# Performance work log

Measured on AMD Instinct MI355X. Metric: run time of the kernel, lower is better.

## Reference

```python
import jax, jax.numpy as jnp
import numpy as np

D_MODEL = 1024
N_HEADS = 16
D_K = D_MODEL // N_HEADS
B, S = 2, 2048


def setup_inputs() -> dict:
    key = jax.random.key(0)
    ks = jax.random.split(key, 5)
    x = jax.random.normal(ks[0], (B, S, D_MODEL), dtype=jnp.float32)
    # causal 0/1 mask, broadcastable over batch and heads
    mask = jnp.tril(jnp.ones((S, S), dtype=jnp.int32))[None, None, :, :]
    scale = 1.0 / np.sqrt(D_MODEL)
    w_qkv_w = jax.random.normal(ks[1], (3 * D_MODEL, D_MODEL), dtype=jnp.float32) * scale
    w_qkv_b = jnp.zeros((3 * D_MODEL,), dtype=jnp.float32)
    w_o_w = jax.random.normal(ks[2], (D_MODEL, D_MODEL), dtype=jnp.float32) * scale
    w_o_b = jnp.zeros((D_MODEL,), dtype=jnp.float32)
    return {"x": x, "mask": mask, "w_qkv_w": w_qkv_w, "w_qkv_b": w_qkv_b,
            "w_o_w": w_o_w, "w_o_b": w_o_b}


def reference(x, mask, w_qkv_w, w_qkv_b, w_o_w, w_o_b):
    b, s, d = x.shape
    qkv = x @ w_qkv_w.T + w_qkv_b                       # [b, s, 3d]
    q, k, v = jnp.split(qkv, 3, axis=-1)
    # [b, h, s, dk]
    q = q.reshape(b, s, N_HEADS, D_K).transpose(0, 2, 1, 3)
    k = k.reshape(b, s, N_HEADS, D_K).transpose(0, 2, 1, 3)
    v = v.reshape(b, s, N_HEADS, D_K).transpose(0, 2, 1, 3)
    scores = jnp.einsum('bhqd,bhkd->bhqk', q, k) / jnp.sqrt(jnp.float32(D_K))
    scores = jnp.where(mask == 0, jnp.float32(-1e9), scores)
    attn = jax.nn.softmax(scores, axis=-1)
    out = jnp.einsum('bhqk,bhkd->bhqd', attn, v)        # [b, h, s, dk]
    out = out.transpose(0, 2, 1, 3).reshape(b, s, d)
    return out @ w_o_w.T + w_o_b
```

## Files before the change

kernel.cpp:

```cpp
#include <hip/hip_runtime.h>
#include <cstdint>
#include <cstddef>


typedef __attribute__((ext_vector_type(8))) short bf16x8;
typedef __attribute__((ext_vector_type(4))) float f32x4;
typedef __attribute__((ext_vector_type(4))) unsigned int u32x4;
typedef __attribute__((ext_vector_type(4))) unsigned short u16x4;
typedef __attribute__((ext_vector_type(8))) unsigned short u16x8;

__device__ __forceinline__ unsigned short f2b(float f) {
  unsigned int u = __float_as_uint(f);
  u = u + 0x7FFFu + ((u >> 16) & 1u);
  return (unsigned short)(u >> 16);
}
__device__ __forceinline__ unsigned short f2b_trunc(float f) {
  return (unsigned short)(__float_as_uint(f) >> 16);
}

__device__ __forceinline__ void gl_lds16(const unsigned short* g, unsigned short* s) {
  __builtin_amdgcn_global_load_lds((const __attribute__((address_space(1))) void*)g,
                                   (__attribute__((address_space(3))) void*)s, 16, 0, 0);
}

__global__ __launch_bounds__(256) void cvt_all(const float* __restrict__ x,
                                               const float* __restrict__ wq,
                                               const float* __restrict__ wo,
                                               unsigned short* __restrict__ xb,
                                               unsigned short* __restrict__ wqb,
                                               unsigned short* __restrict__ wob) {
  const int bid = blockIdx.x;
  const float* in;
  unsigned short* out;
  int base;
  if (bid < 4096)      { in = x;  out = xb;  base = bid; }
  else if (bid < 7168) { in = wq; out = wqb; base = bid - 4096; }
  else                 { in = wo; out = wob; base = bid - 7168; }
  const int idx = (base * 256 + threadIdx.x) * 4;
  f32x4 v = *(const f32x4*)(in + idx);
  u16x4 r;
  r[0] = f2b(v[0]); r[1] = f2b(v[1]); r[2] = f2b(v[2]); r[3] = f2b(v[3]);
  *(u16x4*)(out + idx) = r;
}

__global__ __launch_bounds__(256) void gemm_bt(const unsigned short* __restrict__ A,
                                               const unsigned short* __restrict__ W,
                                               const float* __restrict__ bias,
                                               unsigned short* __restrict__ Cb,
                                               int M, int N, int K, int qcols) {
  __shared__ unsigned short As[2][128 * 32];
  __shared__ unsigned short Bs[2][128 * 32];
  const int tid  = threadIdx.x;
  const int lane = tid & 63;
  const int w    = tid >> 6;
  const int wy   = w >> 1, wx = w & 1;
  const int l15  = lane & 15, quad = lane >> 4;
  const int xr2  = (l15 >> 1) & 3;
  const int m0 = blockIdx.y * 128, n0 = blockIdx.x * 128;

  const unsigned short* gA[2];
  const unsigned short* gB[2];
  int off[2];
#pragma unroll
  for (int p = 0; p < 2; ++p) {
    const int c = tid + p * 256;
    const int r = c >> 2;
    const int srcc = (c & 3) ^ ((r >> 1) & 3);
    gA[p] = A + (size_t)(m0 + r) * K + srcc * 8;
    gB[p] = W + (size_t)(n0 + r) * K + srcc * 8;
    off[p] = c * 8;
  }

  f32x4 acc[4][4];
#pragma unroll
  for (int i = 0; i < 4; ++i)
#pragma unroll
    for (int j = 0; j < 4; ++j) acc[i][j] = (f32x4){0.f, 0.f, 0.f, 0.f};

#pragma unroll
  for (int p = 0; p < 2; ++p) {
    gl_lds16(gA[p], &As[0][off[p]]);
    gl_lds16(gB[p], &Bs[0][off[p]]);
  }

  const int NIT = K >> 5;
  for (int it = 0; it < NIT; ++it) {
    __syncthreads();
    const int cur = it & 1;
    if (it + 1 < NIT) {
      const int kt = (it + 1) << 5;
#pragma unroll
      for (int p = 0; p < 2; ++p) {
        gl_lds16(gA[p] + kt, &As[cur ^ 1][off[p]]);
        gl_lds16(gB[p] + kt, &Bs[cur ^ 1][off[p]]);
      }
    }
    const unsigned short* Ac = As[cur];
    const unsigned short* Bc = Bs[cur];
    bf16x8 af[4], bfr[4];
#pragma unroll
    for (int i = 0; i < 4; ++i)
      af[i] = *(const bf16x8*)&Ac[(wy * 64 + i * 16 + l15) * 32 + (quad ^ xr2) * 8];
#pragma unroll
    for (int j = 0; j < 4; ++j)
      bfr[j] = *(const bf16x8*)&Bc[(wx * 64 + j * 16 + l15) * 32 + (quad ^ xr2) * 8];
#pragma unroll
    for (int i = 0; i < 4; ++i)
#pragma unroll
      for (int j = 0; j < 4; ++j)
        acc[i][j] = __builtin_amdgcn_mfma_f32_16x16x32_bf16(af[i], bfr[j], acc[i][j], 0, 0, 0);
  }

#pragma unroll
  for (int i = 0; i < 4; ++i) {
    const int row = m0 + wy * 64 + i * 16 + quad * 4;
#pragma unroll
    for (int j = 0; j < 4; ++j) {
      const int col = n0 + wx * 64 + j * 16 + l15;
      const float bv = bias[col];
      const float sc = (col < qcols) ? 0.125f : 1.0f;
#pragma unroll
      for (int r = 0; r < 4; ++r)
        Cb[(size_t)(row + r) * N + col] = f2b((acc[i][j][r] + bv) * sc);
    }
  }
}

__global__ __launch_bounds__(256) void gemm_bt64(const unsigned short* __restrict__ A,
                                                 const unsigned short* __restrict__ W,
                                                 const float* __restrict__ bias,
                                                 float* __restrict__ Cf,
                                                 int M, int N, int K) {
  __shared__ unsigned short As[2][64 * 32];
  __shared__ unsigned short Bs[2][64 * 32];
  const int tid  = threadIdx.x;
  const int lane = tid & 63;
  const int w    = tid >> 6;
  const int wy   = w >> 1, wx = w & 1;
  const int l15  = lane & 15, quad = lane >> 4;
  const int xr2  = (l15 >> 1) & 3;
  const int m0 = blockIdx.y * 64, n0 = blockIdx.x * 64;

  const unsigned short* gA0;
  const unsigned short* gB0;
  int off0;
  {
    const int c = tid;
    const int r = c >> 2;
    const int srcc = (c & 3) ^ ((r >> 1) & 3);
    gA0 = A + (size_t)(m0 + r) * K + srcc * 8;
    gB0 = W + (size_t)(n0 + r) * K + srcc * 8;
    off0 = c * 8;
  }

  f32x4 acc[2][2];
#pragma unroll
  for (int i = 0; i < 2; ++i)
#pragma unroll
    for (int j = 0; j < 2; ++j) acc[i][j] = (f32x4){0.f, 0.f, 0.f, 0.f};

  gl_lds16(gA0, &As[0][off0]);
  gl_lds16(gB0, &Bs[0][off0]);

  const int NIT = K >> 5;
  for (int it = 0; it < NIT; ++it) {
    __syncthreads();
    const int cur = it & 1;
    if (it + 1 < NIT) {
      const int kt = (it + 1) << 5;
      gl_lds16(gA0 + kt, &As[cur ^ 1][off0]);
      gl_lds16(gB0 + kt, &Bs[cur ^ 1][off0]);
    }
    const unsigned short* Ac = As[cur];
    const unsigned short* Bc = Bs[cur];
    bf16x8 af[2], bfr[2];
#pragma unroll
    for (int i = 0; i < 2; ++i)
      af[i] = *(const bf16x8*)&Ac[(wy * 32 + i * 16 + l15) * 32 + (quad ^ xr2) * 8];
#pragma unroll
    for (int j = 0; j < 2; ++j)
      bfr[j] = *(const bf16x8*)&Bc[(wx * 32 + j * 16 + l15) * 32 + (quad ^ xr2) * 8];
#pragma unroll
    for (int i = 0; i < 2; ++i)
#pragma unroll
      for (int j = 0; j < 2; ++j)
        acc[i][j] = __builtin_amdgcn_mfma_f32_16x16x32_bf16(af[i], bfr[j], acc[i][j], 0, 0, 0);
  }

#pragma unroll
  for (int i = 0; i < 2; ++i) {
    const int row = m0 + wy * 32 + i * 16 + quad * 4;
#pragma unroll
    for (int j = 0; j < 2; ++j) {
      const int col = n0 + wx * 32 + j * 16 + l15;
      const float bv = bias[col];
#pragma unroll
      for (int r = 0; r < 4; ++r)
        Cf[(size_t)(row + r) * N + col] = acc[i][j][r] + bv;
    }
  }
}

__global__ __launch_bounds__(256) void transpose_v(const unsigned short* __restrict__ qkv,
                                                   unsigned short* __restrict__ vt) {
  __shared__ unsigned short tile[64][72];
  const int tid = threadIdx.x;
  const int bh = blockIdx.y, b = bh >> 4, h = bh & 15;
  const int s0 = blockIdx.x * 64;
  const int i = tid >> 2;
  const int j = (tid & 3) * 16;
  const unsigned short* g = qkv + (size_t)(b * 2048 + s0 + i) * 3072 + 2048 + h * 64 + j;
  *(u32x4*)&tile[i][j]     = *(const u32x4*)g;
  *(u32x4*)&tile[i][j + 8] = *(const u32x4*)(g + 8);
  __syncthreads();
  const int d  = tid >> 2;
  const int sj = (tid & 3) * 16;
  u16x8 o0, o1;
#pragma unroll
  for (int k = 0; k < 8; ++k) { o0[k] = tile[sj + k][d]; o1[k] = tile[sj + 8 + k][d]; }
  unsigned short* gout = vt + (size_t)(bh * 64 + d) * 2048 + s0 + sj;
  *(u16x8*)gout       = o0;
  *(u16x8*)(gout + 8) = o1;
}

__global__ __launch_bounds__(64, 2) void attn_fwd(const unsigned short* __restrict__ qkv,
                                                  const unsigned short* __restrict__ vt,
                                                  unsigned short* __restrict__ o) {
  __shared__ unsigned short Ks[2][64 * 64];
  __shared__ unsigned short P[16 * 72];
  const int lane = threadIdx.x;
  const int l15 = lane & 15, quad = lane >> 4;
  const int xr = l15 & 7;
  const int bh = blockIdx.x, b = bh >> 4, h = bh & 15;
  const int qt = 63 - (int)blockIdx.y;
  const int q0 = qt * 32;
  const int T = (qt >> 1) + 1;

  const unsigned short* gK[8];
#pragma unroll
  for (int p = 0; p < 8; ++p) {
    const int c = p * 64 + lane;
    const int r = c >> 3;
    const int sc = ((c & 7) ^ (r & 7)) * 8;
    gK[p] = qkv + (size_t)(b * 2048 + r) * 3072 + 1024 + h * 64 + sc;
  }

  const unsigned short* qr0 = qkv + (size_t)(b * 2048 + q0 + l15) * 3072 + h * 64;
  const unsigned short* qr1 = qr0 + (size_t)16 * 3072;
  const bf16x8 bq[2][2] = {
    { *(const bf16x8*)(qr0 + quad * 8), *(const bf16x8*)(qr0 + 32 + quad * 8) },
    { *(const bf16x8*)(qr1 + quad * 8), *(const bf16x8*)(qr1 + 32 + quad * 8) } };

  const unsigned short* gV = vt + (size_t)(bh * 64) * 2048;

  bf16x8 vones;
#pragma unroll
  for (int k = 0; k < 8; ++k) vones[k] = (short)0x3F80;

  f32x4 acc[2][4];
#pragma unroll
  for (int i = 0; i < 2; ++i)
#pragma unroll
    for (int j = 0; j < 4; ++j) acc[i][j] = (f32x4){0.f, 0.f, 0.f, 0.f};
  f32x4 accL[2] = {(f32x4){0.f, 0.f, 0.f, 0.f}, (f32x4){0.f, 0.f, 0.f, 0.f}};

#pragma unroll
  for (int p = 0; p < 8; ++p) gl_lds16(gK[p], &Ks[0][p * 512]);

  for (int t = 0; t < T; ++t) {
    __syncthreads();
    const int cur = t & 1;
    const int kv0 = t * 64;
    bf16x8 av[4][2];
#pragma unroll
    for (int j = 0; j < 4; ++j) {
      const unsigned short* vrow = gV + (size_t)(j * 16 + l15) * 2048 + kv0;
      av[j][0] = *(const bf16x8*)(vrow + quad * 8);
      av[j][1] = *(const bf16x8*)(vrow + 32 + quad * 8);
    }
    if (t + 1 < T) {
      const size_t ko = (size_t)(t + 1) * 64 * 3072;
#pragma unroll
      for (int p = 0; p < 8; ++p) gl_lds16(gK[p] + ko, &Ks[cur ^ 1][p * 512]);
    }
    const unsigned short* Kc = Ks[cur];
    bf16x8 kA[4][2];
#pragma unroll
    for (int n = 0; n < 4; ++n) {
      const int row = n * 16 + l15;
      kA[n][0] = *(const bf16x8*)&Kc[row * 64 + ((quad) ^ xr) * 8];
      kA[n][1] = *(const bf16x8*)&Kc[row * 64 + ((4 + quad) ^ xr) * 8];
    }
#pragma unroll
    for (int qs = 0; qs < 2; ++qs) {
      f32x4 st[4];
#pragma unroll
      for (int n = 0; n < 4; ++n) {
        f32x4 z = (f32x4){0.f, 0.f, 0.f, 0.f};
        z = __builtin_amdgcn_mfma_f32_16x16x32_bf16(kA[n][0], bq[qs][0], z, 0, 0, 0);
        z = __builtin_amdgcn_mfma_f32_16x16x32_bf16(kA[n][1], bq[qs][1], z, 0, 0, 0);
        st[n] = z;
      }
      const int qbase = q0 + qs * 16;
      if (kv0 + 63 > qbase) {
        const int qrow = qbase + l15;
#pragma unroll
        for (int n = 0; n < 4; ++n)
#pragma unroll
          for (int r = 0; r < 4; ++r)
            if (kv0 + n * 16 + quad * 4 + r > qrow) st[n][r] = -1e30f;
      }
#pragma unroll
      for (int n = 0; n < 4; ++n) {
#pragma unroll
        for (int r = 0; r < 4; ++r) st[n][r] = __expf(st[n][r]);
        u16x4 pw;
        pw[0] = f2b_trunc(st[n][0]); pw[1] = f2b_trunc(st[n][1]);
        pw[2] = f2b_trunc(st[n][2]); pw[3] = f2b_trunc(st[n][3]);
        *(u16x4*)&P[l15 * 72 + n * 16 + quad * 4] = pw;
      }
      const bf16x8 bp0 = *(const bf16x8*)&P[l15 * 72 + quad * 8];
      const bf16x8 bp1 = *(const bf16x8*)&P[l15 * 72 + 32 + quad * 8];
      accL[qs] = __builtin_amdgcn_mfma_f32_16x16x32_bf16(vones, bp0, accL[qs], 0, 0, 0);
      accL[qs] = __builtin_amdgcn_mfma_f32_16x16x32_bf16(vones, bp1, accL[qs], 0, 0, 0);
#pragma unroll
      for (int j = 0; j < 4; ++j) {
        acc[qs][j] = __builtin_amdgcn_mfma_f32_16x16x32_bf16(av[j][0], bp0, acc[qs][j], 0, 0, 0);
        acc[qs][j] = __builtin_amdgcn_mfma_f32_16x16x32_bf16(av[j][1], bp1, acc[qs][j], 0, 0, 0);
      }
    }
  }
#pragma unroll
  for (int qs = 0; qs < 2; ++qs) {
    const int qrow = q0 + qs * 16 + l15;
    const float inv = 1.0f / accL[qs][0];
    unsigned short* orow = o + (size_t)(b * 2048 + qrow) * 1024 + h * 64;
#pragma unroll
    for (int j = 0; j < 4; ++j) {
      u16x4 ov;
      ov[0] = f2b(acc[qs][j][0] * inv); ov[1] = f2b(acc[qs][j][1] * inv);
      ov[2] = f2b(acc[qs][j][2] * inv); ov[3] = f2b(acc[qs][j][3] * inv);
      *(u16x4*)(orow + j * 16 + quad * 4) = ov;
    }
  }
}

extern "C" void kernel_launch(void* const* d_in, const int* in_sizes, int n_in,
                              void* d_out, int out_size, void* d_ws, size_t ws_size,
                              hipStream_t stream) {
  const float* x       = (const float*)d_in[0];
  const float* w_qkv_w = (const float*)d_in[2];
  const float* w_qkv_b = (const float*)d_in[3];
  const float* w_o_w   = (const float*)d_in[4];
  const float* w_o_b   = (const float*)d_in[5];
  float* out = (float*)d_out;

  unsigned short* ws    = (unsigned short*)d_ws;
  unsigned short* xb    = ws;
  unsigned short* wqb   = xb   + (size_t)4096 * 1024;
  unsigned short* wob   = wqb  + (size_t)3072 * 1024;
  unsigned short* qkvb  = wob  + (size_t)1024 * 1024;
  unsigned short* vtb   = qkvb + (size_t)4096 * 3072;
  unsigned short* attnb = vtb  + (size_t)2048 * 2048;

  cvt_all<<<8192, 256, 0, stream>>>(x, w_qkv_w, w_o_w, xb, wqb, wob);
  gemm_bt<<<dim3(24, 32), 256, 0, stream>>>(xb, wqb, w_qkv_b, qkvb, 4096, 3072, 1024, 1024);
  transpose_v<<<dim3(32, 32), 256, 0, stream>>>(qkvb, vtb);
  attn_fwd<<<dim3(32, 64), 64, 0, stream>>>(qkvb, vtb, attnb);
  gemm_bt64<<<dim3(16, 64), 256, 0, stream>>>(attnb, wob, w_o_b, out, 4096, 1024, 1024);
}
```

Before: 201.6 us.

## Software-pipeline QK^T scores one tile ahead of softmax and PV

Restructures the attention KV loop so the QK^T MFMAs for tile t are issued in the same iteration as the exp/P-write/PV MFMAs for tile t-1. This lets the scheduler overlap matrix work with the exp and LDS traffic of the previous tile. The loop runs one extra iteration and carries 32 extra float registers for the held-over scores, which raises register pressure and may lower occupancy. The V loads are also shifted to the lagged tile.

Measured after the change: 204.6 us. No clear change (+1.5%).

```diff
diff --git a/kernel.cpp b/kernel.cpp
--- a/kernel.cpp
+++ b/kernel.cpp
@@ -264,70 +264,89 @@
     for (int j = 0; j < 4; ++j) acc[i][j] = (f32x4){0.f, 0.f, 0.f, 0.f};
   f32x4 accL[2] = {(f32x4){0.f, 0.f, 0.f, 0.f}, (f32x4){0.f, 0.f, 0.f, 0.f}};
 
+  f32x4 st_old[2][4];
+
 #pragma unroll
   for (int p = 0; p < 8; ++p) gl_lds16(gK[p], &Ks[0][p * 512]);
 
-  for (int t = 0; t < T; ++t) {
+  for (int t = 0; t <= T; ++t) {
     __syncthreads();
     const int cur = t & 1;
-    const int kv0 = t * 64;
+    const bool have_cur = (t < T);
+    const bool have_def = (t >= 1);
+    const int kv0p = (t - 1) * 64;
+
     bf16x8 av[4][2];
-#pragma unroll
-    for (int j = 0; j < 4; ++j) {
-      const unsigned short* vrow = gV + (size_t)(j * 16 + l15) * 2048 + kv0;
-      av[j][0] = *(const bf16x8*)(vrow + quad * 8);
-      av[j][1] = *(const bf16x8*)(vrow + 32 + quad * 8);
+    if (have_def) {
+#pragma unroll
+      for (int j = 0; j < 4; ++j) {
+        const unsigned short* vrow = gV + (size_t)(j * 16 + l15) * 2048 + kv0p;
+        av[j][0] = *(const bf16x8*)(vrow + quad * 8);
+        av[j][1] = *(const bf16x8*)(vrow + 32 + quad * 8);
+      }
     }
     if (t + 1 < T) {
       const size_t ko = (size_t)(t + 1) * 64 * 3072;
 #pragma unroll
       for (int p = 0; p < 8; ++p) gl_lds16(gK[p] + ko, &Ks[cur ^ 1][p * 512]);
     }
-    const unsigned short* Kc = Ks[cur];
-    bf16x8 kA[4][2];
-#pragma unroll
-    for (int n = 0; n < 4; ++n) {
-      const int row = n * 16 + l15;
-      kA[n][0] = *(const bf16x8*)&Kc[row * 64 + ((quad) ^ xr) * 8];
-      kA[n][1] = *(const bf16x8*)&Kc[row * 64 + ((4 + quad) ^ xr) * 8];
-    }
-#pragma unroll
-    for (int qs = 0; qs < 2; ++qs) {
-      f32x4 st[4];
+    f32x4 stn[2][4];
+    if (have_cur) {
+      const unsigned short* Kc = Ks[cur];
+      bf16x8 kA[4][2];
 #pragma unroll
       for (int n = 0; n < 4; ++n) {
-        f32x4 z = (f32x4){0.f, 0.f, 0.f, 0.f};
-        z = __builtin_amdgcn_mfma_f32_16x16x32_bf16(kA[n][0], bq[qs][0], z, 0, 0, 0);
-        z = __builtin_amdgcn_mfma_f32_16x16x32_bf16(kA[n][1], bq[qs][1], z, 0, 0, 0);
-        st[n] = z;
+        const int row = n * 16 + l15;
+        kA[n][0] = *(const bf16x8*)&Kc[row * 64 + ((quad) ^ xr) * 8];
+        kA[n][1] = *(const bf16x8*)&Kc[row * 64 + ((4 + quad) ^ xr) * 8];
       }
-      const int qbase = q0 + qs * 16;
-      if (kv0 + 63 > qbase) {
-        const int qrow = qbase + l15;
-#pragma unroll
-        for (int n = 0; n < 4; ++n)
-#pragma unroll
-          for (int r = 0; r < 4; ++r)
-            if (kv0 + n * 16 + quad * 4 + r > qrow) st[n][r] = -1e30f;
+#pragma unroll
+      for (int qs = 0; qs < 2; ++qs)
+#pragma unroll
+        for (int n = 0; n < 4; ++n) {
+          f32x4 z = (f32x4){0.f, 0.f, 0.f, 0.f};
+          z = __builtin_amdgcn_mfma_f32_16x16x32_bf16(kA[n][0], bq[qs][0], z, 0, 0, 0);
+          z = __builtin_amdgcn_mfma_f32_16x16x32_bf16(kA[n][1], bq[qs][1], z, 0, 0, 0);
+          stn[qs][n] = z;
+        }
+    }
+    if (have_def) {
+#pragma unroll
+      for (int qs = 0; qs < 2; ++qs) {
+        const int qbase = q0 + qs * 16;
+        if (kv0p + 63 > qbase) {
+          const int qrow = qbase + l15;
+#pragma unroll
+          for (int n = 0; n < 4; ++n)
+#pragma unroll
+            for (int r = 0; r < 4; ++r)
+              if (kv0p + n * 16 + quad * 4 + r > qrow) st_old[qs][n][r] = -1e30f;
+        }
+#pragma unroll
+        for (int n = 0; n < 4; ++n) {
+#pragma unroll
+          for (int r = 0; r < 4; ++r) st_old[qs][n][r] = __expf(st_old[qs][n][r]);
+          u16x4 pw;
+          pw[0] = f2b_trunc(st_old[qs][n][0]); pw[1] = f2b_trunc(st_old[qs][n][1]);
+          pw[2] = f2b_trunc(st_old[qs][n][2]); pw[3] = f2b_trunc(st_old[qs][n][3]);
+          *(u16x4*)&P[l15 * 72 + n * 16 + quad * 4] = pw;
+        }
+        const bf16x8 bp0 = *(const bf16x8*)&P[l15 * 72 + quad * 8];
+        const bf16x8 bp1 = *(const bf16x8*)&P[l15 * 72 + 32 + quad * 8];
+        accL[qs] = __builtin_amdgcn_mfma_f32_16x16x32_bf16(vones, bp0, accL[qs], 0, 0, 0);
+        accL[qs] = __builtin_amdgcn_mfma_f32_16x16x32_bf16(vones, bp1, accL[qs], 0, 0, 0);
+#pragma unroll
+        for (int j = 0; j < 4; ++j) {
+          acc[qs][j] = __builtin_amdgcn_mfma_f32_16x16x32_bf16(av[j][0], bp0, acc[qs][j], 0, 0, 0);
+          acc[qs][j] = __builtin_amdgcn_mfma_f32_16x16x32_bf16(av[j][1], bp1, acc[qs][j], 0, 0, 0);
+        }
       }
-#pragma unroll
-      for (int n = 0; n < 4; ++n) {
-#pragma unroll
-        for (int r = 0; r < 4; ++r) st[n][r] = __expf(st[n][r]);
-        u16x4 pw;
-        pw[0] = f2b_trunc(st[n][0]); pw[1] = f2b_trunc(st[n][1]);
-        pw[2] = f2b_trunc(st[n][2]); pw[3] = f2b_trunc(st[n][3]);
-        *(u16x4*)&P[l15 * 72 + n * 16 + quad * 4] = pw;
-      }
-      const bf16x8 bp0 = *(const bf16x8*)&P[l15 * 72 + quad * 8];
-      const bf16x8 bp1 = *(const bf16x8*)&P[l15 * 72 + 32 + quad * 8];
-      accL[qs] = __builtin_amdgcn_mfma_f32_16x16x32_bf16(vones, bp0, accL[qs], 0, 0, 0);
-      accL[qs] = __builtin_amdgcn_mfma_f32_16x16x32_bf16(vones, bp1, accL[qs], 0, 0, 0);
-#pragma unroll
-      for (int j = 0; j < 4; ++j) {
-        acc[qs][j] = __builtin_amdgcn_mfma_f32_16x16x32_bf16(av[j][0], bp0, acc[qs][j], 0, 0, 0);
-        acc[qs][j] = __builtin_amdgcn_mfma_f32_16x16x32_bf16(av[j][1], bp1, acc[qs][j], 0, 0, 0);
-      }
+    }
+    if (have_cur) {
+#pragma unroll
+      for (int qs = 0; qs < 2; ++qs)
+#pragma unroll
+        for (int n = 0; n < 4; ++n) st_old[qs][n] = stn[qs][n];
     }
   }
 #pragma unroll
```

## Fuse V transpose into QKV GEMM epilogue and split attention KV across warps

Applied to the files above, without the earlier changes.

The QKV GEMM epilogue now writes V blocks directly in transposed layout, which removes the separate transpose kernel launch and its extra memory pass. The attention kernel goes from one wave per block to four waves. Each wave handles a strided subset of KV tiles and loads K straight from global memory instead of through double-buffered LDS. Partial accumulators and row sums are then reduced through shared memory. This is meant to add parallelism and hide latency for causal query tiles, at the cost of uncoalesced K loads and a reduction step.

Result: slower. 223.6 us (+10.9%).

```diff
diff --git a/kernel.cpp b/kernel.cpp
--- a/kernel.cpp
+++ b/kernel.cpp
@@ -47,6 +47,7 @@
                                                const unsigned short* __restrict__ W,
                                                const float* __restrict__ bias,
                                                unsigned short* __restrict__ Cb,
+                                               unsigned short* __restrict__ vtb,
                                                int M, int N, int K, int qcols) {
   __shared__ unsigned short As[2][128 * 32];
   __shared__ unsigned short Bs[2][128 * 32];
@@ -111,6 +112,7 @@
         acc[i][j] = __builtin_amdgcn_mfma_f32_16x16x32_bf16(af[i], bfr[j], acc[i][j], 0, 0, 0);
   }
 
+  const bool vblock = (n0 >= 2048);
 #pragma unroll
   for (int i = 0; i < 4; ++i) {
     const int row = m0 + wy * 64 + i * 16 + quad * 4;
@@ -118,10 +120,19 @@
     for (int j = 0; j < 4; ++j) {
       const int col = n0 + wx * 64 + j * 16 + l15;
       const float bv = bias[col];
-      const float sc = (col < qcols) ? 0.125f : 1.0f;
-#pragma unroll
-      for (int r = 0; r < 4; ++r)
-        Cb[(size_t)(row + r) * N + col] = f2b((acc[i][j][r] + bv) * sc);
+      if (!vblock) {
+        const float sc = (col < qcols) ? 0.125f : 1.0f;
+#pragma unroll
+        for (int r = 0; r < 4; ++r)
+          Cb[(size_t)(row + r) * N + col] = f2b((acc[i][j][r] + bv) * sc);
+      } else {
+        const int hd = col - 2048;
+        const int bb = row >> 11, s = row & 2047;
+        u16x4 ov;
+#pragma unroll
+        for (int r = 0; r < 4; ++r) ov[r] = f2b(acc[i][j][r] + bv);
+        *(u16x4*)(vtb + ((size_t)(bb * 1024 + hd)) * 2048 + s) = ov;
+      }
     }
   }
 }
@@ -201,49 +212,19 @@
   }
 }
 
-__global__ __launch_bounds__(256) void transpose_v(const unsigned short* __restrict__ qkv,
-                                                   unsigned short* __restrict__ vt) {
-  __shared__ unsigned short tile[64][72];
-  const int tid = threadIdx.x;
-  const int bh = blockIdx.y, b = bh >> 4, h = bh & 15;
-  const int s0 = blockIdx.x * 64;
-  const int i = tid >> 2;
-  const int j = (tid & 3) * 16;
-  const unsigned short* g = qkv + (size_t)(b * 2048 + s0 + i) * 3072 + 2048 + h * 64 + j;
-  *(u32x4*)&tile[i][j]     = *(const u32x4*)g;
-  *(u32x4*)&tile[i][j + 8] = *(const u32x4*)(g + 8);
-  __syncthreads();
-  const int d  = tid >> 2;
-  const int sj = (tid & 3) * 16;
-  u16x8 o0, o1;
-#pragma unroll
-  for (int k = 0; k < 8; ++k) { o0[k] = tile[sj + k][d]; o1[k] = tile[sj + 8 + k][d]; }
-  unsigned short* gout = vt + (size_t)(bh * 64 + d) * 2048 + s0 + sj;
-  *(u16x8*)gout       = o0;
-  *(u16x8*)(gout + 8) = o1;
-}
-
-__global__ __launch_bounds__(64, 2) void attn_fwd(const unsigned short* __restrict__ qkv,
-                                                  const unsigned short* __restrict__ vt,
-                                                  unsigned short* __restrict__ o) {
-  __shared__ unsigned short Ks[2][64 * 64];
-  __shared__ unsigned short P[16 * 72];
-  const int lane = threadIdx.x;
-  const int l15 = lane & 15, quad = lane >> 4;
-  const int xr = l15 & 7;
+__global__ __launch_bounds__(256, 3) void attn_fwd(const unsigned short* __restrict__ qkv,
+                                                   const unsigned short* __restrict__ vt,
+                                                   unsigned short* __restrict__ o) {
+  __shared__ unsigned short pbuf[4][16 * 72];
+  __shared__ f32x4 red[3][64][10];
+  const int tid  = threadIdx.x;
+  const int lane = tid & 63;
+  const int w    = tid >> 6;
+  const int l15  = lane & 15, quad = lane >> 4;
   const int bh = blockIdx.x, b = bh >> 4, h = bh & 15;
   const int qt = 63 - (int)blockIdx.y;
   const int q0 = qt * 32;
   const int T = (qt >> 1) + 1;
-
-  const unsigned short* gK[8];
-#pragma unroll
-  for (int p = 0; p < 8; ++p) {
-    const int c = p * 64 + lane;
-    const int r = c >> 3;
-    const int sc = ((c & 7) ^ (r & 7)) * 8;
-    gK[p] = qkv + (size_t)(b * 2048 + r) * 3072 + 1024 + h * 64 + sc;
-  }
 
   const unsigned short* qr0 = qkv + (size_t)(b * 2048 + q0 + l15) * 3072 + h * 64;
   const unsigned short* qr1 = qr0 + (size_t)16 * 3072;
@@ -251,6 +232,7 @@
     { *(const bf16x8*)(qr0 + quad * 8), *(const bf16x8*)(qr0 + 32 + quad * 8) },
     { *(const bf16x8*)(qr1 + quad * 8), *(const bf16x8*)(qr1 + 32 + quad * 8) } };
 
+  const unsigned short* gK = qkv + (size_t)(b * 2048) * 3072 + 1024 + h * 64;
   const unsigned short* gV = vt + (size_t)(bh * 64) * 2048;
 
   bf16x8 vones;
@@ -264,32 +246,23 @@
     for (int j = 0; j < 4; ++j) acc[i][j] = (f32x4){0.f, 0.f, 0.f, 0.f};
   f32x4 accL[2] = {(f32x4){0.f, 0.f, 0.f, 0.f}, (f32x4){0.f, 0.f, 0.f, 0.f}};
 
-#pragma unroll
-  for (int p = 0; p < 8; ++p) gl_lds16(gK[p], &Ks[0][p * 512]);
-
-  for (int t = 0; t < T; ++t) {
-    __syncthreads();
-    const int cur = t & 1;
+  unsigned short* P = pbuf[w];
+
+  for (int t = w; t < T; t += 4) {
     const int kv0 = t * 64;
+    bf16x8 kA[4][2];
+#pragma unroll
+    for (int n = 0; n < 4; ++n) {
+      const unsigned short* krow = gK + (size_t)(kv0 + n * 16 + l15) * 3072;
+      kA[n][0] = *(const bf16x8*)(krow + quad * 8);
+      kA[n][1] = *(const bf16x8*)(krow + 32 + quad * 8);
+    }
     bf16x8 av[4][2];
 #pragma unroll
     for (int j = 0; j < 4; ++j) {
       const unsigned short* vrow = gV + (size_t)(j * 16 + l15) * 2048 + kv0;
       av[j][0] = *(const bf16x8*)(vrow + quad * 8);
       av[j][1] = *(const bf16x8*)(vrow + 32 + quad * 8);
-    }
-    if (t + 1 < T) {
-      const size_t ko = (size_t)(t + 1) * 64 * 3072;
-#pragma unroll
-      for (int p = 0; p < 8; ++p) gl_lds16(gK[p] + ko, &Ks[cur ^ 1][p * 512]);
-    }
-    const unsigned short* Kc = Ks[cur];
-    bf16x8 kA[4][2];
-#pragma unroll
-    for (int n = 0; n < 4; ++n) {
-      const int row = n * 16 + l15;
-      kA[n][0] = *(const bf16x8*)&Kc[row * 64 + ((quad) ^ xr) * 8];
-      kA[n][1] = *(const bf16x8*)&Kc[row * 64 + ((4 + quad) ^ xr) * 8];
     }
 #pragma unroll
     for (int qs = 0; qs < 2; ++qs) {
@@ -330,17 +303,44 @@
       }
     }
   }
-#pragma unroll
-  for (int qs = 0; qs < 2; ++qs) {
-    const int qrow = q0 + qs * 16 + l15;
-    const float inv = 1.0f / accL[qs][0];
-    unsigned short* orow = o + (size_t)(b * 2048 + qrow) * 1024 + h * 64;
-#pragma unroll
-    for (int j = 0; j < 4; ++j) {
-      u16x4 ov;
-      ov[0] = f2b(acc[qs][j][0] * inv); ov[1] = f2b(acc[qs][j][1] * inv);
-      ov[2] = f2b(acc[qs][j][2] * inv); ov[3] = f2b(acc[qs][j][3] * inv);
-      *(u16x4*)(orow + j * 16 + quad * 4) = ov;
+
+  if (w > 0) {
+    f32x4* dst = red[w - 1][lane];
+#pragma unroll
+    for (int qs = 0; qs < 2; ++qs)
+#pragma unroll
+      for (int j = 0; j < 4; ++j) dst[qs * 4 + j] = acc[qs][j];
+    dst[8] = (f32x4){accL[0][0], accL[1][0], 0.f, 0.f};
+  }
+  __syncthreads();
+  if (w == 0) {
+#pragma unroll
+    for (int p = 0; p < 3; ++p) {
+      const f32x4* src = red[p][lane];
+#pragma unroll
+      for (int qs = 0; qs < 2; ++qs)
+#pragma unroll
+        for (int j = 0; j < 4; ++j) {
+          const f32x4 s = src[qs * 4 + j];
+#pragma unroll
+          for (int r = 0; r < 4; ++r) acc[qs][j][r] += s[r];
+        }
+      const f32x4 ls = src[8];
+      accL[0][0] += ls[0];
+      accL[1][0] += ls[1];
+    }
+#pragma unroll
+    for (int qs = 0; qs < 2; ++qs) {
+      const int qrow = q0 + qs * 16 + l15;
+      const float inv = 1.0f / accL[qs][0];
+      unsigned short* orow = o + (size_t)(b * 2048 + qrow) * 1024 + h * 64;
+#pragma unroll
+      for (int j = 0; j < 4; ++j) {
+        u16x4 ov;
+        ov[0] = f2b(acc[qs][j][0] * inv); ov[1] = f2b(acc[qs][j][1] * inv);
+        ov[2] = f2b(acc[qs][j][2] * inv); ov[3] = f2b(acc[qs][j][3] * inv);
+        *(u16x4*)(orow + j * 16 + quad * 4) = ov;
+      }
     }
   }
 }
@@ -364,8 +364,7 @@
   unsigned short* attnb = vtb  + (size_t)2048 * 2048;
 
   cvt_all<<<8192, 256, 0, stream>>>(x, w_qkv_w, w_o_w, xb, wqb, wob);
-  gemm_bt<<<dim3(24, 32), 256, 0, stream>>>(xb, wqb, w_qkv_b, qkvb, 4096, 3072, 1024, 1024);
-  transpose_v<<<dim3(32, 32), 256, 0, stream>>>(qkvb, vtb);
-  attn_fwd<<<dim3(32, 64), 64, 0, stream>>>(qkvb, vtb, attnb);
+  gemm_bt<<<dim3(24, 32), 256, 0, stream>>>(xb, wqb, w_qkv_b, qkvb, vtb, 4096, 3072, 1024, 1024);
+  attn_fwd<<<dim3(32, 64), 256, 0, stream>>>(qkvb, vtb, attnb);
   gemm_bt64<<<dim3(16, 64), 256, 0, stream>>>(attnb, wob, w_o_b, out, 4096, 1024, 1024);
 }
```
